# Kernel optimization log

Measured on AMD Instinct MI355X. Metric: run time of the kernel, lower is better.

The kernel has to match this reference:

```python
import jax, jax.numpy as jnp
import numpy as np

B, T, C = 2, 2048, 1024
N_HEAD = 16
HEAD_DIM = C // N_HEAD


def setup_inputs() -> dict:
    key = jax.random.key(0)
    k1, k2, k3 = jax.random.split(key, 3)
    s = 1.0 / np.sqrt(C)
    return {
        "x": jax.random.normal(k1, (B, T, C), dtype=jnp.float32),
        "w_qkv": jax.random.normal(k2, (C, 3 * C), dtype=jnp.float32) * s,
        "b_qkv": jnp.zeros((3 * C,), dtype=jnp.float32),
        "w_out": jax.random.normal(k3, (C, C), dtype=jnp.float32) * s,
        "b_out": jnp.zeros((C,), dtype=jnp.float32),
    }


def reference(x, w_qkv, b_qkv, w_out, b_out):
    b, t, c = x.shape
    qkv = x @ w_qkv + b_qkv                                   # [B,T,3C]
    # Faithful to torch: view(B,T,H,3*hd).transpose(1,2) then split last dim
    qkv = qkv.reshape(b, t, N_HEAD, 3 * HEAD_DIM).transpose(0, 2, 1, 3)  # [B,H,T,3hd]
    q, k, v = jnp.split(qkv, 3, axis=-1)                      # each [B,H,T,hd]
    att = jnp.einsum("bhqd,bhkd->bhqk", q, k) / np.sqrt(HEAD_DIM)
    causal = jnp.tril(jnp.ones((t, t), dtype=bool))
    att = jnp.where(causal[None, None], att, -jnp.inf)
    att = jax.nn.softmax(att, axis=-1)                        # dropout p=0 (eval)
    y = jnp.einsum("bhqk,bhkd->bhqd", att, v)                 # [B,H,T,hd]
    y = y.transpose(0, 2, 1, 3).reshape(b, t, c)
    return y @ w_out + b_out
```

## Files before the change

kernel.cpp:

```cpp
#include <hip/hip_runtime.h>


#define T_SEQ 2048
#define C_DIM 1024
#define NH    16
#define HD    64
#define BT    4096

typedef short bf16x8 __attribute__((ext_vector_type(8)));
typedef float floatx4 __attribute__((ext_vector_type(4)));

static __device__ __forceinline__ unsigned short f2bf(float f) {
    union { float f; unsigned u; } v; v.f = f;
    unsigned u = v.u;
    return (unsigned short)((u + 0x7FFFu + ((u >> 16) & 1u)) >> 16);
}
static __device__ __forceinline__ float bf2f(unsigned short u) {
    union { unsigned u; float f; } v; v.u = ((unsigned)u) << 16; return v.f;
}

static __device__ __forceinline__ void gl2lds16(const void* g, void* l) {
    __builtin_amdgcn_global_load_lds(
        (const __attribute__((address_space(1))) unsigned int*)g,
        (__attribute__((address_space(3))) unsigned int*)l, 16, 0, 0);
}

static __device__ __forceinline__ void transpose_body(float (*tile)[65],
                                                      const float* __restrict__ W,
                                                      unsigned short* __restrict__ Wt,
                                                      int K, int N, int bx, int by) {
    const int k0 = by << 6;
    const int n0 = bx << 6;
    const int rr = threadIdx.x >> 4;
    const int cc = (threadIdx.x & 15) << 2;
#pragma unroll
    for (int i = 0; i < 4; i++) {
        int r = rr + (i << 4);
        *(float4*)&tile[r][cc] = *(const float4*)(W + (size_t)(k0 + r) * N + n0 + cc);
    }
    __syncthreads();
#pragma unroll
    for (int i = 0; i < 4; i++) {
        int nr = rr + (i << 4);
        ushort4 o;
        o.x = f2bf(tile[cc + 0][nr]);
        o.y = f2bf(tile[cc + 1][nr]);
        o.z = f2bf(tile[cc + 2][nr]);
        o.w = f2bf(tile[cc + 3][nr]);
        *(ushort4*)(Wt + (size_t)(n0 + nr) * K + k0 + cc) = o;
    }
}

__global__ __launch_bounds__(256) void prep(const float* __restrict__ x,
                                            unsigned short* __restrict__ xb,
                                            const float* __restrict__ w_qkv,
                                            unsigned short* __restrict__ wqkvT,
                                            const float* __restrict__ w_out,
                                            unsigned short* __restrict__ woutT) {
    __shared__ float tile[64][65];
    const int bx = blockIdx.x;
    if (bx < 1024) {
        int i = (bx * 256 + threadIdx.x) * 4;
        const int n = BT * C_DIM;
        const int stride = 1024 * 1024;
        for (; i < n; i += stride) {
            float4 f = *(const float4*)(x + i);
            ushort4 o;
            o.x = f2bf(f.x); o.y = f2bf(f.y); o.z = f2bf(f.z); o.w = f2bf(f.w);
            *(ushort4*)(xb + i) = o;
        }
    } else if (bx < 1024 + 768) {
        int b = bx - 1024;
        transpose_body(tile, w_qkv, wqkvT, 1024, 3072, b % 48, b / 48);
    } else {
        int b = bx - 1024 - 768;
        transpose_body(tile, w_out, woutT, 1024, 1024, b % 16, b / 16);
    }
}

__global__ __launch_bounds__(256) void transp_v(const unsigned short* __restrict__ vb,
                                                unsigned short* __restrict__ vt) {
    __shared__ unsigned short tile[64][68];
    const int t0 = blockIdx.x << 6;
    const int bh = blockIdx.y;
    const size_t base = (size_t)bh * T_SEQ * HD;
    const int r = threadIdx.x >> 3;
    const int c = (threadIdx.x & 7) << 3;
#pragma unroll
    for (int i = 0; i < 2; i++) {
        const unsigned short* src = vb + base + (size_t)(t0 + r + (i << 5)) * HD + c;
        ushort4 u0 = *(const ushort4*)src;
        ushort4 u1 = *(const ushort4*)(src + 4);
        *(ushort4*)&tile[r + (i << 5)][c] = u0;
        *(ushort4*)&tile[r + (i << 5)][c + 4] = u1;
    }
    __syncthreads();
#pragma unroll
    for (int i = 0; i < 2; i++) {
        int s = threadIdx.x + (i << 8);
        int d = s >> 3;
        int tc = (s & 7) << 3;
        ushort4 o0, o1;
        o0.x = tile[tc + 0][d]; o0.y = tile[tc + 1][d];
        o0.z = tile[tc + 2][d]; o0.w = tile[tc + 3][d];
        o1.x = tile[tc + 4][d]; o1.y = tile[tc + 5][d];
        o1.z = tile[tc + 6][d]; o1.w = tile[tc + 7][d];
        unsigned short* dst = vt + ((size_t)bh * HD + d) * T_SEQ + t0 + tc;
        *(ushort4*)dst = o0;
        *(ushort4*)(dst + 4) = o1;
    }
}

#define GEMM_CORE(A_, Bt_, K_)                                                      \
    __shared__ short As[128 * 64];                                                  \
    __shared__ short Bs[128 * 64];                                                  \
    const int tid  = threadIdx.x;                                                   \
    const int lane = tid & 63, wave = tid >> 6;                                     \
    const int ln   = lane & 15, quad = lane >> 4;                                   \
    const int wm   = wave & 1,  wn   = wave >> 1;                                   \
    const int row0 = blockIdx.y << 7;                                               \
    const int col0 = blockIdx.x << 7;                                               \
    floatx4 acc[4][4];                                                              \
    _Pragma("unroll")                                                               \
    for (int i = 0; i < 4; i++)                                                     \
        _Pragma("unroll")                                                           \
        for (int j = 0; j < 4; j++) acc[i][j] = (floatx4){0.f, 0.f, 0.f, 0.f};      \
    for (int k0 = 0; k0 < K_; k0 += 64) {                                           \
        _Pragma("unroll")                                                           \
        for (int i = 0; i < 4; i++) {                                               \
            int c = (i << 8) + tid;                                                 \
            int r = c >> 3;                                                         \
            int gsrc = (c & 7) ^ (r & 7);                                           \
            gl2lds16(A_  + (size_t)(row0 + r) * K_ + k0 + (gsrc << 3), &As[c << 3]); \
            gl2lds16(Bt_ + (size_t)(col0 + r) * K_ + k0 + (gsrc << 3), &Bs[c << 3]); \
        }                                                                           \
        __syncthreads();                                                            \
        _Pragma("unroll")                                                           \
        for (int half = 0; half < 2; half++) {                                      \
            bf16x8 af[4], bfr[4];                                                   \
            _Pragma("unroll")                                                       \
            for (int t4 = 0; t4 < 4; t4++) {                                        \
                int ra = (wm << 6) + (t4 << 4) + ln;                                \
                int rb = (wn << 6) + (t4 << 4) + ln;                                \
                int g  = (half << 2) + quad;                                        \
                af[t4]  = *(bf16x8*)&As[((ra << 3) + (g ^ (ra & 7))) << 3];         \
                bfr[t4] = *(bf16x8*)&Bs[((rb << 3) + (g ^ (rb & 7))) << 3];         \
            }                                                                       \
            _Pragma("unroll")                                                       \
            for (int mt = 0; mt < 4; mt++)                                          \
                _Pragma("unroll")                                                   \
                for (int nt = 0; nt < 4; nt++)                                      \
                    acc[mt][nt] = __builtin_amdgcn_mfma_f32_16x16x32_bf16(af[mt], bfr[nt], acc[mt][nt], 0, 0, 0); \
        }                                                                           \
        __syncthreads();                                                            \
    }

__global__ __launch_bounds__(256) void gemm_qkv(const unsigned short* __restrict__ A,
                                                const unsigned short* __restrict__ Bt,
                                                const float* __restrict__ bias,
                                                unsigned short* __restrict__ qb,
                                                unsigned short* __restrict__ kb,
                                                unsigned short* __restrict__ vb) {
    GEMM_CORE(A, Bt, 1024)
#pragma unroll
    for (int mt = 0; mt < 4; mt++) {
#pragma unroll
        for (int nt = 0; nt < 4; nt++) {
            int n = col0 + (wn << 6) + (nt << 4) + ln;
            int h = n / 192, r = n % 192;
            int sel = r >> 6, d = r & 63;
            float bv = bias[n];
#pragma unroll
            for (int e = 0; e < 4; e++) {
                int m = row0 + (wm << 6) + (mt << 4) + (quad << 2) + e;
                int b = m >> 11, t = m & 2047;
                float val = acc[mt][nt][e] + bv;
                size_t idx = (((size_t)(b * NH + h)) * T_SEQ + t) * HD + d;
                if (sel == 0)
                    qb[idx] = f2bf(val * 0.125f);
                else if (sel == 1)
                    kb[idx] = f2bf(val);
                else
                    vb[idx] = f2bf(val);
            }
        }
    }
}

__global__ __launch_bounds__(256) void gemm_out(const unsigned short* __restrict__ A,
                                                const unsigned short* __restrict__ Bt,
                                                const float* __restrict__ bias,
                                                float* __restrict__ out) {
    const int K = 1024, N = 1024;
    __shared__ short As[128 * 64];
    __shared__ short Bs[64 * 64];
    const int tid  = threadIdx.x;
    const int lane = tid & 63, wave = tid >> 6;
    const int ln   = lane & 15, quad = lane >> 4;
    const int wm   = wave & 1,  wn   = wave >> 1;
    const int row0 = blockIdx.y << 7;
    const int col0 = blockIdx.x << 6;
    floatx4 acc[4][2];
#pragma unroll
    for (int i = 0; i < 4; i++)
#pragma unroll
        for (int j = 0; j < 2; j++) acc[i][j] = (floatx4){0.f, 0.f, 0.f, 0.f};
    for (int k0 = 0; k0 < K; k0 += 64) {
#pragma unroll
        for (int i = 0; i < 4; i++) {
            int c = (i << 8) + tid;
            int r = c >> 3;
            int gsrc = (c & 7) ^ (r & 7);
            gl2lds16(A + (size_t)(row0 + r) * K + k0 + (gsrc << 3), &As[c << 3]);
        }
#pragma unroll
        for (int i = 0; i < 2; i++) {
            int c = (i << 8) + tid;
            int r = c >> 3;
            int gsrc = (c & 7) ^ (r & 7);
            gl2lds16(Bt + (size_t)(col0 + r) * K + k0 + (gsrc << 3), &Bs[c << 3]);
        }
        __syncthreads();
#pragma unroll
        for (int half = 0; half < 2; half++) {
            bf16x8 af[4], bfr[2];
#pragma unroll
            for (int t4 = 0; t4 < 4; t4++) {
                int ra = (wm << 6) + (t4 << 4) + ln;
                int g  = (half << 2) + quad;
                af[t4] = *(bf16x8*)&As[((ra << 3) + (g ^ (ra & 7))) << 3];
            }
#pragma unroll
            for (int t2 = 0; t2 < 2; t2++) {
                int rb = (wn << 5) + (t2 << 4) + ln;
                int g  = (half << 2) + quad;
                bfr[t2] = *(bf16x8*)&Bs[((rb << 3) + (g ^ (rb & 7))) << 3];
            }
#pragma unroll
            for (int mt = 0; mt < 4; mt++)
#pragma unroll
                for (int nt = 0; nt < 2; nt++)
                    acc[mt][nt] = __builtin_amdgcn_mfma_f32_16x16x32_bf16(af[mt], bfr[nt], acc[mt][nt], 0, 0, 0);
        }
        __syncthreads();
    }
#pragma unroll
    for (int mt = 0; mt < 4; mt++) {
#pragma unroll
        for (int nt = 0; nt < 2; nt++) {
            int n = col0 + (wn << 5) + (nt << 4) + ln;
            float bv = bias[n];
#pragma unroll
            for (int e = 0; e < 4; e++) {
                int m = row0 + (wm << 6) + (mt << 4) + (quad << 2) + e;
                out[(size_t)m * N + n] = acc[mt][nt][e] + bv;
            }
        }
    }
}

__global__ __launch_bounds__(256, 4) void attn_p1(const unsigned short* __restrict__ qb,
                                                  const unsigned short* __restrict__ kb,
                                                  const unsigned short* __restrict__ vt,
                                                  unsigned short* __restrict__ y,
                                                  unsigned short* __restrict__ po,
                                                  float* __restrict__ pm,
                                                  float* __restrict__ pl) {
    __shared__ short Ks[64][72];
    __shared__ short Vs[64][72];
    __shared__ short QP[64][72];
    const int tid  = threadIdx.x;
    const int w    = tid >> 6, lane = tid & 63;
    const int ln   = lane & 15, quad = lane >> 4;
    const int bx   = blockIdx.x;
    int qt, cidx, kt_lo; bool fin;
    if (bx < 16)      { qt = 31 - bx;        cidx = 0; kt_lo = 0;  fin = false; }
    else if (bx < 32) { qt = 31 - (bx - 16); cidx = 1; kt_lo = 16; fin = false; }
    else              { qt = 15 - (bx - 32); cidx = 0; kt_lo = 0;  fin = true;  }
    const int kt_hi = (!fin && cidx == 0) ? 15 : qt;
    const int bh   = blockIdx.y;
    const size_t base = (size_t)bh * T_SEQ * HD;
    const int q0   = qt << 6;
    const int sb   = q0 + (w << 4);
    const float NEG_INF = -__builtin_inff();

    const int sr = tid >> 3;
    const int sc = (tid & 7) << 3;

    bf16x8 qtmp[2], kreg[2], vreg[2];
    const int kk0 = kt_lo << 6;
#pragma unroll
    for (int i = 0; i < 2; i++) {
        qtmp[i] = *(const bf16x8*)(qb + base + (size_t)(q0 + sr + (i << 5)) * HD + sc);
        kreg[i] = *(const bf16x8*)(kb + base + (size_t)(kk0 + sr + (i << 5)) * HD + sc);
        vreg[i] = *(const bf16x8*)(vt + base + (size_t)(sr + (i << 5)) * T_SEQ + kk0 + sc);
    }
#pragma unroll
    for (int i = 0; i < 2; i++) *(bf16x8*)&QP[sr + (i << 5)][sc] = qtmp[i];
    __syncthreads();

    bf16x8 bq0 = *(bf16x8*)&QP[(w << 4) + ln][quad << 3];
    bf16x8 bq1 = *(bf16x8*)&QP[(w << 4) + ln][32 + (quad << 3)];

    floatx4 o[4];
#pragma unroll
    for (int nt = 0; nt < 4; nt++) o[nt] = (floatx4){0.f, 0.f, 0.f, 0.f};
    float m_prev = NEG_INF, l_run = 0.f;

    for (int kt = kt_lo; kt <= kt_hi; kt++) {
        const int k0 = kt << 6;
        __syncthreads();
#pragma unroll
        for (int i = 0; i < 2; i++) {
            *(bf16x8*)&Ks[sr + (i << 5)][sc] = kreg[i];
            *(bf16x8*)&Vs[sr + (i << 5)][sc] = vreg[i];
        }
        __syncthreads();
        if (kt < kt_hi) {
            const int kn = k0 + 64;
#pragma unroll
            for (int i = 0; i < 2; i++) {
                kreg[i] = *(const bf16x8*)(kb + base + (size_t)(kn + sr + (i << 5)) * HD + sc);
                vreg[i] = *(const bf16x8*)(vt + base + (size_t)(sr + (i << 5)) * T_SEQ + kn + sc);
            }
        }

        const bool diag  = (kt == qt);
        const int  nlive = diag ? w : 3;

        floatx4 st[4];
#pragma unroll
        for (int ktl = 0; ktl < 4; ktl++) {
            if (ktl <= nlive) {
                bf16x8 a0 = *(bf16x8*)&Ks[(ktl << 4) + ln][quad << 3];
                bf16x8 a1 = *(bf16x8*)&Ks[(ktl << 4) + ln][32 + (quad << 3)];
                floatx4 acc = (floatx4){0.f, 0.f, 0.f, 0.f};
                acc = __builtin_amdgcn_mfma_f32_16x16x32_bf16(a0, bq0, acc, 0, 0, 0);
                acc = __builtin_amdgcn_mfma_f32_16x16x32_bf16(a1, bq1, acc, 0, 0, 0);
                st[ktl] = acc;
            }
        }
        if (diag) {
#pragma unroll
            for (int ktl = 0; ktl < 4; ktl++) {
                if (ktl <= nlive) {
#pragma unroll
                    for (int e = 0; e < 4; e++) {
                        int kg = k0 + (ktl << 4) + (quad << 2) + e;
                        if (kg > sb + ln) st[ktl][e] = NEG_INF;
                    }
                }
            }
        }

        float mx = NEG_INF;
#pragma unroll
        for (int ktl = 0; ktl < 4; ktl++)
            if (ktl <= nlive) {
#pragma unroll
                for (int e = 0; e < 4; e++) mx = fmaxf(mx, st[ktl][e]);
            }
        mx = fmaxf(mx, __shfl_xor(mx, 16));
        mx = fmaxf(mx, __shfl_xor(mx, 32));
        float m_new = fmaxf(m_prev, mx);
        float alpha = __expf(m_prev - m_new);
        float psum = 0.f;
#pragma unroll
        for (int ktl = 0; ktl < 4; ktl++)
            if (ktl <= nlive) {
#pragma unroll
                for (int e = 0; e < 4; e++) {
                    float p = __expf(st[ktl][e] - m_new);
                    st[ktl][e] = p;
                    psum += p;
                }
            }
        psum += __shfl_xor(psum, 16);
        psum += __shfl_xor(psum, 32);
        l_run = l_run * alpha + psum;
        m_prev = m_new;

#pragma unroll
        for (int ktl = 0; ktl < 4; ktl++) {
            ushort4 pw;
            if (ktl <= nlive) {
                pw.x = f2bf(st[ktl][0]); pw.y = f2bf(st[ktl][1]);
                pw.z = f2bf(st[ktl][2]); pw.w = f2bf(st[ktl][3]);
            } else {
                pw.x = 0; pw.y = 0; pw.z = 0; pw.w = 0;
            }
            *(ushort4*)&QP[(w << 4) + ln][(ktl << 4) + (quad << 2)] = pw;
        }

        float arow[4];
#pragma unroll
        for (int e = 0; e < 4; e++) arow[e] = __shfl(alpha, (quad << 2) + e);
#pragma unroll
        for (int nt = 0; nt < 4; nt++)
#pragma unroll
            for (int e = 0; e < 4; e++) o[nt][e] *= arow[e];

        bf16x8 ap0 = *(bf16x8*)&QP[(w << 4) + ln][quad << 3];
        bf16x8 ap1 = *(bf16x8*)&QP[(w << 4) + ln][32 + (quad << 3)];
#pragma unroll
        for (int nt = 0; nt < 4; nt++) {
            bf16x8 v0 = *(bf16x8*)&Vs[(nt << 4) + ln][quad << 3];
            bf16x8 v1 = *(bf16x8*)&Vs[(nt << 4) + ln][32 + (quad << 3)];
            o[nt] = __builtin_amdgcn_mfma_f32_16x16x32_bf16(ap0, v0, o[nt], 0, 0, 0);
            o[nt] = __builtin_amdgcn_mfma_f32_16x16x32_bf16(ap1, v1, o[nt], 0, 0, 0);
        }
    }

    if (fin) {
        float linv[4];
#pragma unroll
        for (int e = 0; e < 4; e++) linv[e] = 1.0f / __shfl(l_run, (quad << 2) + e);
        const int b = bh >> 4, h = bh & 15;
#pragma unroll
        for (int e = 0; e < 4; e++) {
            int t = sb + (quad << 2) + e;
            unsigned short* yrow = y + ((size_t)b * T_SEQ + t) * C_DIM + h * HD;
#pragma unroll
            for (int nt = 0; nt < 4; nt++)
                yrow[(nt << 4) + ln] = f2bf(o[nt][e] * linv[e]);
        }
    } else {
        const int slot = (((bh << 4) + (qt - 16)) << 1) + cidx;
        if (quad == 0) {
            pm[(slot << 6) + (w << 4) + ln] = m_prev;
            pl[(slot << 6) + (w << 4) + ln] = l_run;
        }
#pragma unroll
        for (int e = 0; e < 4; e++) {
            int q = (w << 4) + (quad << 2) + e;
            unsigned short* porow = po + (((size_t)slot << 6) + q) * HD;
#pragma unroll
            for (int nt = 0; nt < 4; nt++)
                porow[(nt << 4) + ln] = f2bf(o[nt][e]);
        }
    }
}

__global__ __launch_bounds__(256) void attn_p2(const unsigned short* __restrict__ po,
                                               const float* __restrict__ pm,
                                               const float* __restrict__ pl,
                                               unsigned short* __restrict__ y) {
    const int qt = 16 + blockIdx.x;
    const int bh = blockIdx.y;
    const int slot0 = ((bh << 4) + (qt - 16)) << 1;
    const int tid = threadIdx.x;
    const int q  = tid >> 2;
    const int d0 = (tid & 3) << 4;
    float m0 = pm[(slot0 << 6) + q], m1 = pm[((slot0 + 1) << 6) + q];
    float l0 = pl[(slot0 << 6) + q], l1 = pl[((slot0 + 1) << 6) + q];
    float m  = fmaxf(m0, m1);
    float a0 = __expf(m0 - m), a1 = __expf(m1 - m);
    float inv = 1.0f / (l0 * a0 + l1 * a1);
    a0 *= inv; a1 *= inv;
    const unsigned short* r0 = po + (((size_t)slot0 << 6) + q) * HD + d0;
    const unsigned short* r1 = po + (((size_t)(slot0 + 1) << 6) + q) * HD + d0;
    const int b = bh >> 4, h = bh & 15;
    const int t = (qt << 6) + q;
    unsigned short* yrow = y + ((size_t)b * T_SEQ + t) * C_DIM + h * HD + d0;
#pragma unroll
    for (int i = 0; i < 4; i++) {
        ushort4 u0 = *(const ushort4*)(r0 + (i << 2));
        ushort4 u1 = *(const ushort4*)(r1 + (i << 2));
        ushort4 ow;
        ow.x = f2bf(bf2f(u0.x) * a0 + bf2f(u1.x) * a1);
        ow.y = f2bf(bf2f(u0.y) * a0 + bf2f(u1.y) * a1);
        ow.z = f2bf(bf2f(u0.z) * a0 + bf2f(u1.z) * a1);
        ow.w = f2bf(bf2f(u0.w) * a0 + bf2f(u1.w) * a1);
        *(ushort4*)(yrow + (i << 2)) = ow;
    }
}

extern "C" void kernel_launch(void* const* d_in, const int* in_sizes, int n_in,
                              void* d_out, int out_size, void* d_ws, size_t ws_size,
                              hipStream_t stream) {
    (void)in_sizes; (void)n_in; (void)out_size; (void)ws_size;
    const float* x     = (const float*)d_in[0];
    const float* w_qkv = (const float*)d_in[1];
    const float* b_qkv = (const float*)d_in[2];
    const float* w_out = (const float*)d_in[3];
    const float* b_out = (const float*)d_in[4];
    float* out = (float*)d_out;

    char* ws = (char*)d_ws;
    unsigned short* qb    = (unsigned short*)ws;
    unsigned short* kb    = (unsigned short*)(ws + ((size_t)8  << 20));
    unsigned short* vb    = (unsigned short*)(ws + ((size_t)16 << 20));
    unsigned short* vt    = (unsigned short*)(ws + ((size_t)24 << 20));
    unsigned short* xb    = (unsigned short*)(ws + ((size_t)32 << 20));
    unsigned short* yb    = xb;
    unsigned short* wqkvT = (unsigned short*)(ws + ((size_t)40 << 20));
    unsigned short* woutT = (unsigned short*)(ws + ((size_t)46 << 20));
    unsigned short* po    = (unsigned short*)(ws + ((size_t)48 << 20));
    float*          pm    = (float*)(ws + ((size_t)56 << 20));
    float*          pl    = (float*)(ws + ((size_t)56 << 20) + (256 << 10));

    prep    <<<2048, 256, 0, stream>>>(x, xb, w_qkv, wqkvT, w_out, woutT);
    gemm_qkv<<<dim3(24, 32), 256, 0, stream>>>(xb, wqkvT, b_qkv, qb, kb, vb);
    transp_v<<<dim3(32, 32), 256, 0, stream>>>(vb, vt);
    attn_p1 <<<dim3(48, 32), 256, 0, stream>>>(qb, kb, vt, yb, po, pm, pl);
    attn_p2 <<<dim3(16, 32), 256, 0, stream>>>(po, pm, pl, yb);
    gemm_out<<<dim3(16, 32), 256, 0, stream>>>(yb, woutT, b_out, out);
}
```

Measured before the change: 211.0 us.

## Split causal attention into 8-tile KV chunks with a multi-way merge

Attention work is now split into KV chunks of 8 tiles each, so long query tiles use up to 4 partial blocks instead of 2 and the grid grows from 48 to 80 blocks per head. The merge kernel now combines up to 4 partials, with a new slot layout and a rearranged workspace. Q fragments are loaded straight from global memory into registers, which drops the LDS staging step and one barrier. The LDS row padding is reduced and the launch-bounds occupancy hint is raised to 6. The aim is better load balance across the causal triangle and higher occupancy, at the cost of more partial-output traffic. The 68-short row stride may leave 16-byte LDS vector accesses misaligned.

```diff
diff --git a/kernel.cpp b/kernel.cpp
--- a/kernel.cpp
+++ b/kernel.cpp
@@ -259,25 +259,29 @@
     }
 }
 
-__global__ __launch_bounds__(256, 4) void attn_p1(const unsigned short* __restrict__ qb,
+__global__ __launch_bounds__(256, 6) void attn_p1(const unsigned short* __restrict__ qb,
                                                   const unsigned short* __restrict__ kb,
                                                   const unsigned short* __restrict__ vt,
                                                   unsigned short* __restrict__ y,
                                                   unsigned short* __restrict__ po,
                                                   float* __restrict__ pm,
                                                   float* __restrict__ pl) {
-    __shared__ short Ks[64][72];
-    __shared__ short Vs[64][72];
-    __shared__ short QP[64][72];
+    __shared__ short Ks[64][68];
+    __shared__ short Vs[64][68];
+    __shared__ short QP[64][68];
     const int tid  = threadIdx.x;
     const int w    = tid >> 6, lane = tid & 63;
     const int ln   = lane & 15, quad = lane >> 4;
     const int bx   = blockIdx.x;
-    int qt, cidx, kt_lo; bool fin;
-    if (bx < 16)      { qt = 31 - bx;        cidx = 0; kt_lo = 0;  fin = false; }
-    else if (bx < 32) { qt = 31 - (bx - 16); cidx = 1; kt_lo = 16; fin = false; }
-    else              { qt = 15 - (bx - 32); cidx = 0; kt_lo = 0;  fin = true;  }
-    const int kt_hi = (!fin && cidx == 0) ? 15 : qt;
+    int qt, c;
+    if (bx < 32)      { qt = 31 - bx;        c = 0; }
+    else if (bx < 56) { qt = 31 - (bx - 32); c = 1; }
+    else if (bx < 72) { qt = 31 - (bx - 56); c = 2; }
+    else              { qt = 31 - (bx - 72); c = 3; }
+    const int kt_lo = c << 3;
+    const int kt_hi = (kt_lo + 7 < qt) ? (kt_lo + 7) : qt;
+    const int nc    = (qt >> 3) + 1;
+    const bool fin  = (nc == 1);
     const int bh   = blockIdx.y;
     const size_t base = (size_t)bh * T_SEQ * HD;
     const int q0   = qt << 6;
@@ -287,20 +291,17 @@
     const int sr = tid >> 3;
     const int sc = (tid & 7) << 3;
 
-    bf16x8 qtmp[2], kreg[2], vreg[2];
+    const unsigned short* qrow = qb + base + (size_t)(q0 + (w << 4) + ln) * HD;
+    bf16x8 bq0 = *(const bf16x8*)(qrow + (quad << 3));
+    bf16x8 bq1 = *(const bf16x8*)(qrow + 32 + (quad << 3));
+
+    bf16x8 kreg[2], vreg[2];
     const int kk0 = kt_lo << 6;
 #pragma unroll
     for (int i = 0; i < 2; i++) {
-        qtmp[i] = *(const bf16x8*)(qb + base + (size_t)(q0 + sr + (i << 5)) * HD + sc);
         kreg[i] = *(const bf16x8*)(kb + base + (size_t)(kk0 + sr + (i << 5)) * HD + sc);
         vreg[i] = *(const bf16x8*)(vt + base + (size_t)(sr + (i << 5)) * T_SEQ + kk0 + sc);
     }
-#pragma unroll
-    for (int i = 0; i < 2; i++) *(bf16x8*)&QP[sr + (i << 5)][sc] = qtmp[i];
-    __syncthreads();
-
-    bf16x8 bq0 = *(bf16x8*)&QP[(w << 4) + ln][quad << 3];
-    bf16x8 bq1 = *(bf16x8*)&QP[(w << 4) + ln][32 + (quad << 3)];
 
     floatx4 o[4];
 #pragma unroll
@@ -425,7 +426,11 @@
                 yrow[(nt << 4) + ln] = f2bf(o[nt][e] * linv[e]);
         }
     } else {
-        const int slot = (((bh << 4) + (qt - 16)) << 1) + cidx;
+        int cb;
+        if (qt < 16)      cb = (qt - 8) * 2;
+        else if (qt < 24) cb = 16 + (qt - 16) * 3;
+        else              cb = 40 + (qt - 24) * 4;
+        const int slot = bh * 72 + cb + c;
         if (quad == 0) {
             pm[(slot << 6) + (w << 4) + ln] = m_prev;
             pl[(slot << 6) + (w << 4) + ln] = l_run;
@@ -445,32 +450,70 @@
                                                const float* __restrict__ pm,
                                                const float* __restrict__ pl,
                                                unsigned short* __restrict__ y) {
-    const int qt = 16 + blockIdx.x;
+    const int qt = 8 + blockIdx.x;
     const int bh = blockIdx.y;
-    const int slot0 = ((bh << 4) + (qt - 16)) << 1;
+    const int nc = (qt >> 3) + 1;
+    int cb;
+    if (qt < 16)      cb = (qt - 8) * 2;
+    else if (qt < 24) cb = 16 + (qt - 16) * 3;
+    else              cb = 40 + (qt - 24) * 4;
+    const int slot0 = bh * 72 + cb;
     const int tid = threadIdx.x;
     const int q  = tid >> 2;
     const int d0 = (tid & 3) << 4;
-    float m0 = pm[(slot0 << 6) + q], m1 = pm[((slot0 + 1) << 6) + q];
-    float l0 = pl[(slot0 << 6) + q], l1 = pl[((slot0 + 1) << 6) + q];
-    float m  = fmaxf(m0, m1);
-    float a0 = __expf(m0 - m), a1 = __expf(m1 - m);
-    float inv = 1.0f / (l0 * a0 + l1 * a1);
-    a0 *= inv; a1 *= inv;
-    const unsigned short* r0 = po + (((size_t)slot0 << 6) + q) * HD + d0;
-    const unsigned short* r1 = po + (((size_t)(slot0 + 1) << 6) + q) * HD + d0;
+    const float NEG_INF = -__builtin_inff();
+
+    float mv[4], lv[4];
+#pragma unroll
+    for (int cc = 0; cc < 4; cc++) {
+        if (cc < nc) {
+            mv[cc] = pm[((slot0 + cc) << 6) + q];
+            lv[cc] = pl[((slot0 + cc) << 6) + q];
+        } else {
+            mv[cc] = NEG_INF; lv[cc] = 0.f;
+        }
+    }
+    float m = fmaxf(fmaxf(mv[0], mv[1]), fmaxf(mv[2], mv[3]));
+    float a[4];
+    float L = 0.f;
+#pragma unroll
+    for (int cc = 0; cc < 4; cc++) {
+        a[cc] = __expf(mv[cc] - m);
+        L += lv[cc] * a[cc];
+    }
+    const float inv = 1.0f / L;
+#pragma unroll
+    for (int cc = 0; cc < 4; cc++) a[cc] *= inv;
+
+    float acc[16];
+#pragma unroll
+    for (int i = 0; i < 16; i++) acc[i] = 0.f;
+#pragma unroll
+    for (int cc = 0; cc < 4; cc++) {
+        if (cc < nc) {
+            const unsigned short* r = po + (((size_t)(slot0 + cc)) << 12) + (q << 6) + d0;
+            const float ac = a[cc];
+#pragma unroll
+            for (int i = 0; i < 4; i++) {
+                ushort4 u = *(const ushort4*)(r + (i << 2));
+                acc[(i << 2) + 0] += ac * bf2f(u.x);
+                acc[(i << 2) + 1] += ac * bf2f(u.y);
+                acc[(i << 2) + 2] += ac * bf2f(u.z);
+                acc[(i << 2) + 3] += ac * bf2f(u.w);
+            }
+        }
+    }
+
     const int b = bh >> 4, h = bh & 15;
     const int t = (qt << 6) + q;
     unsigned short* yrow = y + ((size_t)b * T_SEQ + t) * C_DIM + h * HD + d0;
 #pragma unroll
     for (int i = 0; i < 4; i++) {
-        ushort4 u0 = *(const ushort4*)(r0 + (i << 2));
-        ushort4 u1 = *(const ushort4*)(r1 + (i << 2));
         ushort4 ow;
-        ow.x = f2bf(bf2f(u0.x) * a0 + bf2f(u1.x) * a1);
-        ow.y = f2bf(bf2f(u0.y) * a0 + bf2f(u1.y) * a1);
-        ow.z = f2bf(bf2f(u0.z) * a0 + bf2f(u1.z) * a1);
-        ow.w = f2bf(bf2f(u0.w) * a0 + bf2f(u1.w) * a1);
+        ow.x = f2bf(acc[(i << 2) + 0]);
+        ow.y = f2bf(acc[(i << 2) + 1]);
+        ow.z = f2bf(acc[(i << 2) + 2]);
+        ow.w = f2bf(acc[(i << 2) + 3]);
         *(ushort4*)(yrow + (i << 2)) = ow;
     }
 }
@@ -489,20 +532,20 @@
     char* ws = (char*)d_ws;
     unsigned short* qb    = (unsigned short*)ws;
     unsigned short* kb    = (unsigned short*)(ws + ((size_t)8  << 20));
-    unsigned short* vb    = (unsigned short*)(ws + ((size_t)16 << 20));
-    unsigned short* vt    = (unsigned short*)(ws + ((size_t)24 << 20));
-    unsigned short* xb    = (unsigned short*)(ws + ((size_t)32 << 20));
+    unsigned short* vt    = (unsigned short*)(ws + ((size_t)16 << 20));
+    unsigned short* xb    = (unsigned short*)(ws + ((size_t)24 << 20));
     unsigned short* yb    = xb;
-    unsigned short* wqkvT = (unsigned short*)(ws + ((size_t)40 << 20));
-    unsigned short* woutT = (unsigned short*)(ws + ((size_t)46 << 20));
-    unsigned short* po    = (unsigned short*)(ws + ((size_t)48 << 20));
-    float*          pm    = (float*)(ws + ((size_t)56 << 20));
-    float*          pl    = (float*)(ws + ((size_t)56 << 20) + (256 << 10));
+    unsigned short* woutT = (unsigned short*)(ws + ((size_t)32 << 20));
+    unsigned short* vb    = (unsigned short*)(ws + ((size_t)34 << 20));
+    unsigned short* wqkvT = (unsigned short*)(ws + ((size_t)42 << 20));
+    unsigned short* po    = (unsigned short*)(ws + ((size_t)34 << 20));
+    float*          pm    = (float*)(ws + ((size_t)52 << 20));
+    float*          pl    = (float*)(ws + ((size_t)52 << 20) + (640 << 10));
 
     prep    <<<2048, 256, 0, stream>>>(x, xb, w_qkv, wqkvT, w_out, woutT);
     gemm_qkv<<<dim3(24, 32), 256, 0, stream>>>(xb, wqkvT, b_qkv, qb, kb, vb);
     transp_v<<<dim3(32, 32), 256, 0, stream>>>(vb, vt);
-    attn_p1 <<<dim3(48, 32), 256, 0, stream>>>(qb, kb, vt, yb, po, pm, pl);
-    attn_p2 <<<dim3(16, 32), 256, 0, stream>>>(po, pm, pl, yb);
+    attn_p1 <<<dim3(80, 32), 256, 0, stream>>>(qb, kb, vt, yb, po, pm, pl);
+    attn_p2 <<<dim3(24, 32), 256, 0, stream>>>(po, pm, pl, yb);
     gemm_out<<<dim3(16, 32), 256, 0, stream>>>(yb, woutT, b_out, out);
 }
```

Result: slower. 245.2 us (+16.2%).
